# Kernel tuning notes

Hardware: AMD Instinct MI355X
Metric: run time of the kernel (lower is better)

Reference implementation:

```python
import jax, jax.numpy as jnp
import numpy as np

NEG = -9e15

def setup_inputs() -> dict:
    key = jax.random.key(0)
    k1, k2, k3, k4, k5, k6 = jax.random.split(key, 6)
    N, Fin, Fout = 8192, 256, 128
    inp = jax.random.normal(k1, (N, Fin), dtype=jnp.float32)
    adj = jax.random.randint(k2, (N, N), 0, 2, dtype=jnp.int32)
    W_w = jax.random.normal(k3, (Fout, Fin), dtype=jnp.float32) / np.sqrt(Fin)
    W_b = jax.random.normal(k4, (Fout,), dtype=jnp.float32) * 0.01
    a_w = jax.random.normal(k5, (1, 2 * Fout), dtype=jnp.float32) / np.sqrt(2 * Fout)
    a_b = jax.random.normal(k6, (1,), dtype=jnp.float32) * 0.01
    return {"input": inp, "adj": adj, "W_w": W_w, "W_b": W_b, "a_w": a_w, "a_b": a_b}

def reference(input, adj, W_w, W_b, a_w, a_b):
    alpha = 0.2
    Fout = W_w.shape[0]
    h = input @ W_w.T + W_b                      # [N, Fout]
    # a([h_i || h_j]) = a1.h_i + a2.h_j + b  (exact decomposition of concat+linear)
    a1 = a_w[0, :Fout]
    a2 = a_w[0, Fout:]
    e = jax.nn.leaky_relu((h @ a1)[:, None] + (h @ a2)[None, :] + a_b[0],
                          negative_slope=alpha)   # [N, N]
    scores = jnp.where(adj > 0, e, NEG)
    attention = jax.nn.softmax(scores, axis=1)    # dropout in eval mode = identity
    h_prime = attention @ h                       # [N, Fout]
    return jax.nn.elu(h_prime)
```

## Files before the change

kernel.cpp:

```cpp
#include <hip/hip_runtime.h>
#include <hip/hip_bf16.h>
#include <cmath>

#define NN 8192
#define FIN 256
#define FOUT 128
#define ROWS 32
#define NCH 4
#define JC (NN / NCH)
#define NWINC (JC / 64)
#define NWIN 8

typedef short short8 __attribute__((ext_vector_type(8)));
typedef float f32x16 __attribute__((ext_vector_type(16)));
typedef unsigned long long u64;

static __device__ __forceinline__ unsigned short f2bf(float f) {
    unsigned u = __float_as_uint(f);
    u += 0x7fffu + ((u >> 16) & 1u);
    return (unsigned short)(u >> 16);
}

__global__ __launch_bounds__(256, 2)
void gat_pass_a(const float* __restrict__ input, const float* __restrict__ W,
                const float* __restrict__ Wb, const float* __restrict__ aw,
                const float* __restrict__ ab, unsigned short* __restrict__ hT3,
                float* __restrict__ s_out, float* __restrict__ t_out) {
    const int tid = threadIdx.x;
    const int w = tid >> 6, l = tid & 63;
    const int l5 = l >> 5, l31 = l & 31;
    const int nt = w >> 1, mh = w & 1;
    const int bx = blockIdx.x;
    const int i = bx * 64 + nt * 32 + l31;

    f32x16 acc0 = {}; f32x16 acc1 = {};
    #pragma unroll
    for (int ks = 0; ks < FIN / 16; ++ks) {
        const int c0 = ks * 16 + l5 * 8;
        const float4 b0 = *(const float4*)(input + (size_t)i * FIN + c0);
        const float4 b1 = *(const float4*)(input + (size_t)i * FIN + c0 + 4);
        short8 bf;
        bf[0]=(short)f2bf(b0.x); bf[1]=(short)f2bf(b0.y); bf[2]=(short)f2bf(b0.z); bf[3]=(short)f2bf(b0.w);
        bf[4]=(short)f2bf(b1.x); bf[5]=(short)f2bf(b1.y); bf[6]=(short)f2bf(b1.z); bf[7]=(short)f2bf(b1.w);
        {
            const int kcol = l31 + 32 * (2 * mh + 0);
            const float4 a0 = *(const float4*)(W + (size_t)kcol * FIN + c0);
            const float4 a1 = *(const float4*)(W + (size_t)kcol * FIN + c0 + 4);
            short8 af;
            af[0]=(short)f2bf(a0.x); af[1]=(short)f2bf(a0.y); af[2]=(short)f2bf(a0.z); af[3]=(short)f2bf(a0.w);
            af[4]=(short)f2bf(a1.x); af[5]=(short)f2bf(a1.y); af[6]=(short)f2bf(a1.z); af[7]=(short)f2bf(a1.w);
            acc0 = __builtin_amdgcn_mfma_f32_32x32x16_bf16(af, bf, acc0, 0, 0, 0);
        }
        {
            const int kcol = l31 + 32 * (2 * mh + 1);
            const float4 a0 = *(const float4*)(W + (size_t)kcol * FIN + c0);
            const float4 a1 = *(const float4*)(W + (size_t)kcol * FIN + c0 + 4);
            short8 af;
            af[0]=(short)f2bf(a0.x); af[1]=(short)f2bf(a0.y); af[2]=(short)f2bf(a0.z); af[3]=(short)f2bf(a0.w);
            af[4]=(short)f2bf(a1.x); af[5]=(short)f2bf(a1.y); af[6]=(short)f2bf(a1.z); af[7]=(short)f2bf(a1.w);
            acc1 = __builtin_amdgcn_mfma_f32_32x32x16_bf16(af, bf, acc1, 0, 0, 0);
        }
    }
    __shared__ float sred[4][32];
    __shared__ float tred[4][32];
    float sacc = 0.f, tacc = 0.f;
    const int jloc = nt * 32 + l31;
    const int ksb = jloc >> 4;
    const int lane_j = 32 * ((jloc >> 3) & 1);
    const int e = jloc & 7;
    #pragma unroll
    for (int m = 0; m < 2; ++m) {
        #pragma unroll
        for (int r = 0; r < 16; ++r) {
            const int kcol = 32 * (2 * mh + m) + 4 * l5 + (r & 3) + 8 * (r >> 2);
            const float hv = (m ? acc1[r] : acc0[r]) + Wb[kcol];
            const int fg = kcol >> 5;
            const int lane = (kcol & 31) + lane_j;
            hT3[((((size_t)bx * 4 + fg) * 4 + ksb) * 64 + lane) * 8 + e] = f2bf(hv);
            sacc += hv * aw[kcol];
            tacc += hv * aw[FOUT + kcol];
        }
    }
    sacc += __shfl_xor(sacc, 32);
    tacc += __shfl_xor(tacc, 32);
    if (l < 32) { sred[w][l] = sacc; tred[w][l] = tacc; }
    __syncthreads();
    if (mh == 0 && l < 32) {
        s_out[i] = sred[w][l] + sred[w + 1][l];
        t_out[i] = tred[w][l] + tred[w + 1][l] + ab[0];
    }
}

__global__ __launch_bounds__(256, 4)
void gat_pass_b(const int* __restrict__ adj, const unsigned short* __restrict__ hT3,
                const float* __restrict__ s_in, const float* __restrict__ t_in,
                float* __restrict__ numw, float* __restrict__ dpart) {
    __shared__ float red[FOUT * ROWS];
    __shared__ float denb[4][ROWS];
    __shared__ u64 mask[ROWS][33];
    const int tid = threadIdx.x;
    const int wv = tid >> 6, l = tid & 63;
    const int l5 = l >> 5, l31 = l & 31;
    const int i0 = blockIdx.x * ROWS;
    const int chunk = blockIdx.y;
    const int jb = chunk * JC;
    const float si = s_in[i0 + l31];

    const int* arow = adj + (size_t)(i0 + wv * 8) * NN + jb + l * 4;
    const int lq = (l & 31) >> 2;
    const int sh = 16 * (l & 3);
    int4 Rc[8];
    #pragma unroll
    for (int q = 0; q < 8; ++q) Rc[q] = *(const int4*)(arow + q * 256);
    #pragma unroll
    for (int rr = 0; rr < 8; ++rr) {
        u64 myword = 0;
        #pragma unroll
        for (int q = 0; q < 8; ++q) {
            const int4 a = Rc[q];
            const u64 b0 = __ballot(a.x > 0);
            const u64 b1 = __ballot(a.y > 0);
            const u64 b2 = __ballot(a.z > 0);
            const u64 b3 = __ballot(a.w > 0);
            if (lq == q) {
                myword = ((b0 >> sh) & 0xFFFFull)
                       | (((b1 >> sh) & 0xFFFFull) << 16)
                       | (((b2 >> sh) & 0xFFFFull) << 32)
                       | (((b3 >> sh) & 0xFFFFull) << 48);
            }
        }
        if (rr < 7) {
            #pragma unroll
            for (int q = 0; q < 8; ++q)
                Rc[q] = *(const int4*)(arow + (size_t)(rr + 1) * NN + q * 256);
        }
        if (l < 32) mask[wv * 8 + rr][l] = myword;
    }
    __syncthreads();

    f32x16 acc0 = {}, acc1 = {}, acc2 = {}, acc3 = {};
    float dacc = 0.f;

    for (int w = 0; w < NWIN; ++w) {
        const int win = wv * NWIN + w;
        const u64 myw = mask[l31][win];
        const int jw = jb + win * 64;
        const int tile = jw >> 6;
        #pragma unroll
        for (int ks = 0; ks < 4; ++ks) {
            const int jsl = jw + ks * 16 + l5 * 8;
            const float4 t0 = *(const float4*)(t_in + jsl);
            const float4 t1 = *(const float4*)(t_in + jsl + 4);
            const u64 m = myw >> (ks * 4 + l5 * 2);
            short8 bf;
            float x, p;
            x = si + t0.x; x = fmaxf(x, 0.2f * x); p = __expf(x);
            p = ((m >> 0)  & 1ull) ? p : 0.f; dacc += p; bf[0] = (short)f2bf(p);
            x = si + t0.y; x = fmaxf(x, 0.2f * x); p = __expf(x);
            p = ((m >> 16) & 1ull) ? p : 0.f; dacc += p; bf[1] = (short)f2bf(p);
            x = si + t0.z; x = fmaxf(x, 0.2f * x); p = __expf(x);
            p = ((m >> 32) & 1ull) ? p : 0.f; dacc += p; bf[2] = (short)f2bf(p);
            x = si + t0.w; x = fmaxf(x, 0.2f * x); p = __expf(x);
            p = ((m >> 48) & 1ull) ? p : 0.f; dacc += p; bf[3] = (short)f2bf(p);
            x = si + t1.x; x = fmaxf(x, 0.2f * x); p = __expf(x);
            p = ((m >> 1)  & 1ull) ? p : 0.f; dacc += p; bf[4] = (short)f2bf(p);
            x = si + t1.y; x = fmaxf(x, 0.2f * x); p = __expf(x);
            p = ((m >> 17) & 1ull) ? p : 0.f; dacc += p; bf[5] = (short)f2bf(p);
            x = si + t1.z; x = fmaxf(x, 0.2f * x); p = __expf(x);
            p = ((m >> 33) & 1ull) ? p : 0.f; dacc += p; bf[6] = (short)f2bf(p);
            x = si + t1.w; x = fmaxf(x, 0.2f * x); p = __expf(x);
            p = ((m >> 49) & 1ull) ? p : 0.f; dacc += p; bf[7] = (short)f2bf(p);

            const unsigned short* hp =
                hT3 + (((size_t)tile * 4) * 4 + ks) * 512 + (size_t)l * 8;
            const short8 af0 = *(const short8*)(hp);
            const short8 af1 = *(const short8*)(hp + 2048);
            const short8 af2 = *(const short8*)(hp + 4096);
            const short8 af3 = *(const short8*)(hp + 6144);
            acc0 = __builtin_amdgcn_mfma_f32_32x32x16_bf16(af0, bf, acc0, 0, 0, 0);
            acc1 = __builtin_amdgcn_mfma_f32_32x32x16_bf16(af1, bf, acc1, 0, 0, 0);
            acc2 = __builtin_amdgcn_mfma_f32_32x32x16_bf16(af2, bf, acc2, 0, 0, 0);
            acc3 = __builtin_amdgcn_mfma_f32_32x32x16_bf16(af3, bf, acc3, 0, 0, 0);
        }
    }

    #pragma unroll
    for (int ph = 0; ph < 4; ++ph) {
        __syncthreads();
        if (wv == ph) {
            #pragma unroll
            for (int r = 0; r < 16; ++r) {
                const int fr = (r & 3) + 8 * (r >> 2) + 4 * l5;
                if (ph == 0) {
                    red[(fr     ) * ROWS + l31] = acc0[r];
                    red[(fr + 32) * ROWS + l31] = acc1[r];
                    red[(fr + 64) * ROWS + l31] = acc2[r];
                    red[(fr + 96) * ROWS + l31] = acc3[r];
                } else {
                    red[(fr     ) * ROWS + l31] += acc0[r];
                    red[(fr + 32) * ROWS + l31] += acc1[r];
                    red[(fr + 64) * ROWS + l31] += acc2[r];
                    red[(fr + 96) * ROWS + l31] += acc3[r];
                }
            }
        }
    }
    dacc += __shfl_xor(dacc, 32);
    if (l5 == 0) denb[wv][l31] = dacc;
    __syncthreads();

    float* nb = numw + (size_t)chunk * FOUT * NN;
    #pragma unroll
    for (int e = 0; e < 4; ++e) {
        const int f = e * 32 + (tid >> 3);
        const int io = (tid & 7) * 4;
        *(float4*)(nb + (size_t)f * NN + i0 + io) = *(const float4*)(red + f * ROWS + io);
    }
    if (tid < ROWS)
        dpart[(size_t)chunk * NN + i0 + tid] =
            denb[0][tid] + denb[1][tid] + denb[2][tid] + denb[3][tid];
}

__global__ __launch_bounds__(256)
void gat_reduce(const float* __restrict__ numw, const float* __restrict__ dpart,
                float* __restrict__ out, int nchunk) {
    __shared__ float tile[FOUT * 33];
    __shared__ float dent[32];
    const int t = threadIdx.x;
    const int i0 = blockIdx.x * 32;
    if (t < 32) {
        float d = 0.f;
        for (int c = 0; c < nchunk; ++c) d += dpart[(size_t)c * NN + i0 + t];
        dent[t] = d;
    }
    __syncthreads();
    #pragma unroll
    for (int e = 0; e < 4; ++e) {
        const int f = e * 32 + (t >> 3);
        const int io = (t & 7) * 4;
        float4 s = {0.f, 0.f, 0.f, 0.f};
        for (int c = 0; c < nchunk; ++c) {
            const float4 v = *(const float4*)(numw + ((size_t)c * FOUT + f) * NN + i0 + io);
            s.x += v.x; s.y += v.y; s.z += v.z; s.w += v.w;
        }
        float v;
        v = s.x / dent[io + 0]; tile[f * 33 + io + 0] = (v > 0.f) ? v : expm1f(v);
        v = s.y / dent[io + 1]; tile[f * 33 + io + 1] = (v > 0.f) ? v : expm1f(v);
        v = s.z / dent[io + 2]; tile[f * 33 + io + 2] = (v > 0.f) ? v : expm1f(v);
        v = s.w / dent[io + 3]; tile[f * 33 + io + 3] = (v > 0.f) ? v : expm1f(v);
    }
    __syncthreads();
    #pragma unroll
    for (int e = 0; e < 4; ++e) {
        const int row = (t >> 5) * 4 + e;
        const int fo = (t & 31) * 4;
        const float4 v = { tile[(fo + 0) * 33 + row], tile[(fo + 1) * 33 + row],
                           tile[(fo + 2) * 33 + row], tile[(fo + 3) * 33 + row] };
        *(float4*)(out + (size_t)(i0 + row) * FOUT + fo) = v;
    }
}

extern "C" void kernel_launch(void* const* d_in, const int* in_sizes, int n_in,
                              void* d_out, int out_size, void* d_ws, size_t ws_size,
                              hipStream_t stream) {
    const float* input = (const float*)d_in[0];
    const int*   adj   = (const int*)d_in[1];
    const float* Ww    = (const float*)d_in[2];
    const float* Wb    = (const float*)d_in[3];
    const float* aw    = (const float*)d_in[4];
    const float* ab    = (const float*)d_in[5];
    float* out = (float*)d_out;

    char* ws = (char*)d_ws;
    unsigned short* hT3 = (unsigned short*)ws;
    float* s_buf = (float*)(ws + (size_t)FOUT * NN * 2);
    float* t_buf = s_buf + NN;
    float* dpart = t_buf + NN;
    float* numw = dpart + (size_t)NCH * NN;

    gat_pass_a<<<dim3(NN / 64), 256, 0, stream>>>(input, Ww, Wb, aw, ab, hT3, s_buf, t_buf);
    gat_pass_b<<<dim3(NN / ROWS, NCH), 256, 0, stream>>>(adj, hT3, s_buf, t_buf, numw, dpart);
    gat_reduce<<<dim3(NN / 32), 256, 0, stream>>>(numw, dpart, out, NCH);
}
```

Before: 106.1 us.

## Split adjacency bitmask compression into a separate kernel before attention pass

Adds a standalone kernel that reads the int32 adjacency matrix once and packs it into 64-bit masks, stored in a blocked layout in workspace. The main attention kernel then loads its per-lane mask words directly from global memory with vector loads. This replaces the in-kernel ballot packing, the shared-memory mask array and its barrier. The aim is to let the bandwidth-heavy adjacency read run as its own fully parallel stream and to lighten the compute kernel, at the cost of an extra launch and a small write/read of the mask buffer.

```diff
diff --git a/kernel.cpp b/kernel.cpp
--- a/kernel.cpp
+++ b/kernel.cpp
@@ -8,7 +8,6 @@
 #define ROWS 32
 #define NCH 4
 #define JC (NN / NCH)
-#define NWINC (JC / 64)
 #define NWIN 8
 
 typedef short short8 __attribute__((ext_vector_type(8)));
@@ -19,6 +18,25 @@
     unsigned u = __float_as_uint(f);
     u += 0x7fffu + ((u >> 16) & 1u);
     return (unsigned short)(u >> 16);
+}
+
+__global__ __launch_bounds__(256)
+void gat_compress(const int* __restrict__ adj, u64* __restrict__ bm3) {
+    const int t = threadIdx.x;
+    const int row = blockIdx.x * 2 + (t >> 7);
+    const int wing = t & 127;
+    const int4* p = (const int4*)(adj + (size_t)row * NN + wing * 64);
+    u64 m = 0;
+    #pragma unroll
+    for (int q = 0; q < 16; ++q) {
+        const int4 v = p[q];
+        m |= (u64)(v.x > 0) << q;
+        m |= (u64)(v.y > 0) << (16 + q);
+        m |= (u64)(v.z > 0) << (32 + q);
+        m |= (u64)(v.w > 0) << (48 + q);
+    }
+    const int ib = row >> 5, r = row & 31, ch = wing >> 5, winc = wing & 31;
+    bm3[((size_t)(ib * 4 + ch)) * 1024 + r * 32 + winc] = m;
 }
 
 __global__ __launch_bounds__(256, 2)
@@ -92,12 +110,11 @@
 }
 
 __global__ __launch_bounds__(256, 4)
-void gat_pass_b(const int* __restrict__ adj, const unsigned short* __restrict__ hT3,
+void gat_pass_b(const u64* __restrict__ bm3, const unsigned short* __restrict__ hT3,
                 const float* __restrict__ s_in, const float* __restrict__ t_in,
                 float* __restrict__ numw, float* __restrict__ dpart) {
     __shared__ float red[FOUT * ROWS];
     __shared__ float denb[4][ROWS];
-    __shared__ u64 mask[ROWS][33];
     const int tid = threadIdx.x;
     const int wv = tid >> 6, l = tid & 63;
     const int l5 = l >> 5, l31 = l & 31;
@@ -106,44 +123,24 @@
     const int jb = chunk * JC;
     const float si = s_in[i0 + l31];
 
-    const int* arow = adj + (size_t)(i0 + wv * 8) * NN + jb + l * 4;
-    const int lq = (l & 31) >> 2;
-    const int sh = 16 * (l & 3);
-    int4 Rc[8];
-    #pragma unroll
-    for (int q = 0; q < 8; ++q) Rc[q] = *(const int4*)(arow + q * 256);
-    #pragma unroll
-    for (int rr = 0; rr < 8; ++rr) {
-        u64 myword = 0;
-        #pragma unroll
-        for (int q = 0; q < 8; ++q) {
-            const int4 a = Rc[q];
-            const u64 b0 = __ballot(a.x > 0);
-            const u64 b1 = __ballot(a.y > 0);
-            const u64 b2 = __ballot(a.z > 0);
-            const u64 b3 = __ballot(a.w > 0);
-            if (lq == q) {
-                myword = ((b0 >> sh) & 0xFFFFull)
-                       | (((b1 >> sh) & 0xFFFFull) << 16)
-                       | (((b2 >> sh) & 0xFFFFull) << 32)
-                       | (((b3 >> sh) & 0xFFFFull) << 48);
-            }
-        }
-        if (rr < 7) {
-            #pragma unroll
-            for (int q = 0; q < 8; ++q)
-                Rc[q] = *(const int4*)(arow + (size_t)(rr + 1) * NN + q * 256);
-        }
-        if (l < 32) mask[wv * 8 + rr][l] = myword;
-    }
-    __syncthreads();
+    const u64* mbase = bm3 + ((size_t)(i0 >> 5) * 4 + chunk) * 1024
+                     + (size_t)l31 * 32 + wv * NWIN;
+    const int4 Rm0 = ((const int4*)mbase)[0];
+    const int4 Rm1 = ((const int4*)mbase)[1];
+    const int4 Rm2 = ((const int4*)mbase)[2];
+    const int4 Rm3 = ((const int4*)mbase)[3];
 
     f32x16 acc0 = {}, acc1 = {}, acc2 = {}, acc3 = {};
     float dacc = 0.f;
 
+    #pragma unroll
     for (int w = 0; w < NWIN; ++w) {
+        const int4 pair = (w >> 1) == 0 ? Rm0 : (w >> 1) == 1 ? Rm1
+                        : (w >> 1) == 2 ? Rm2 : Rm3;
+        const u64 myw = (w & 1)
+            ? (((u64)(unsigned)pair.z) | (((u64)(unsigned)pair.w) << 32))
+            : (((u64)(unsigned)pair.x) | (((u64)(unsigned)pair.y) << 32));
         const int win = wv * NWIN + w;
-        const u64 myw = mask[l31][win];
         const int jw = jb + win * 64;
         const int tile = jw >> 6;
         #pragma unroll
@@ -277,8 +274,10 @@
     float* t_buf = s_buf + NN;
     float* dpart = t_buf + NN;
     float* numw = dpart + (size_t)NCH * NN;
+    u64* bm3 = (u64*)(numw + (size_t)NCH * NN * FOUT);
 
     gat_pass_a<<<dim3(NN / 64), 256, 0, stream>>>(input, Ww, Wb, aw, ab, hT3, s_buf, t_buf);
-    gat_pass_b<<<dim3(NN / ROWS, NCH), 256, 0, stream>>>(adj, hT3, s_buf, t_buf, numw, dpart);
+    gat_compress<<<dim3(NN / 2), 256, 0, stream>>>(adj, bm3);
+    gat_pass_b<<<dim3(NN / ROWS, NCH), 256, 0, stream>>>(bm3, hT3, s_buf, t_buf, numw, dpart);
     gat_reduce<<<dim3(NN / 32), 256, 0, stream>>>(numw, dpart, out, NCH);
 }
```

New measurement: 325.1 us. 206% more time.
